# Optimization experiments

Measured on AMD Instinct MI355X. Metric: run time of the kernel, lower is better.

Reference implementation:

```python
import jax, jax.numpy as jnp
import numpy as np
from jax import lax

B, N, IN_DIM = 8, 196, 2048
C = 256          # conv_channels / subspace dim
G = 1            # relation_glimpse


def _dilated_conv(x, w, b, dil):
    # x: [B,N,N,Cin], w: [3,3,Cin,Cout], SAME padding, rhs dilation per source
    y = lax.conv_general_dilated(x, w, window_strides=(1, 1), padding='SAME',
                                 rhs_dilation=dil,
                                 dimension_numbers=('NHWC', 'HWIO', 'NHWC'))
    return y + b


def _rel_map(X):
    # X: [B,N,N,G] -> symmetric add, move glimpse to axis 1, softmax over N*N
    Xs = X + jnp.transpose(X, (0, 2, 1, 3))          # [B,N,N,G]
    m = jnp.transpose(Xs, (0, 3, 2, 1))              # [B,G,N,N]
    bsz, g, n, _ = m.shape
    m = jax.nn.softmax(m.reshape(bsz, g, n * n), axis=2)
    return m.reshape(bsz, g, n, n)


def setup_inputs() -> dict:
    key = jax.random.key(0)
    ks = jax.random.split(key, 8)
    s = lambda *sh: 1.0 / np.sqrt(sh[-2] if len(sh) > 1 else sh[0])
    return {
        'x': jax.random.normal(ks[0], (B, N, IN_DIM), jnp.float32),
        'w_prj': jax.random.normal(ks[1], (IN_DIM, C), jnp.float32) * 0.02,
        'b_prj': jnp.zeros((C,), jnp.float32),
        'w01': jax.random.normal(ks[2], (C, C // 2), jnp.float32) * 0.06,
        'b01': jnp.zeros((C // 2,), jnp.float32),
        'w02': jax.random.normal(ks[3], (C // 2, C // 4), jnp.float32) * 0.09,
        'b02': jnp.zeros((C // 4,), jnp.float32),
        'w03': jax.random.normal(ks[4], (C // 4, G), jnp.float32) * 0.125,
        'b03': jnp.zeros((G,), jnp.float32),
        'w1': jax.random.normal(ks[5], (3, 3, C, C // 2), jnp.float32) * 0.02,
        'b1': jnp.zeros((C // 2,), jnp.float32),
        'w2': jax.random.normal(ks[6], (3, 3, C // 2, C // 4), jnp.float32) * 0.03,
        'b2': jnp.zeros((C // 4,), jnp.float32),
        'w3': jax.random.normal(ks[7], (3, 3, C // 4, G), jnp.float32) * 0.04,
        'b3': jnp.zeros((G,), jnp.float32),
    }


def reference(x, w_prj, b_prj, w01, b01, w02, b02, w03, b03,
              w1, b1, w2, b2, w3, b3):
    # project to subspace: [B,N,C]
    sub = jnp.einsum('bnd,dc->bnc', x, w_prj) + b_prj
    # pairwise outer product: pair[b,i,j,c] = sub[b,i,c]*sub[b,j,c]
    pair = sub[:, :, None, :] * sub[:, None, :, :]          # [B,N,N,C]

    # branch 0: stacked 1x1 convs (pointwise) with relu; dropout = identity (eval)
    X0 = jax.nn.relu(jnp.einsum('bijc,cd->bijd', pair, w01) + b01)
    X0 = jax.nn.relu(jnp.einsum('bijc,cd->bijd', X0, w02) + b02)
    X0 = jax.nn.relu(jnp.einsum('bijc,cd->bijd', X0, w03) + b03)  # [B,N,N,G]
    rel_map0 = _rel_map(X0)                                  # [B,G,N,N]

    # branch 1: stacked 3x3 dilated convs, dilations (1,1),(1,2),(1,4)
    X1 = jax.nn.relu(_dilated_conv(pair, w1, b1, (1, 1)))
    X1 = jax.nn.relu(_dilated_conv(X1, w2, b2, (1, 2)))
    X1 = jax.nn.relu(_dilated_conv(X1, w3, b3, (1, 4)))      # [B,N,N,G]
    rel_map1 = _rel_map(X1)

    # aggregation over glimpses: rel_x = sum_g (map1[g]@x + map0[g]@x) / (2G)
    rel_x = (jnp.einsum('bgij,bjd->bid', rel_map1, x) +
             jnp.einsum('bgij,bjd->bid', rel_map0, x)) / (2.0 * G)
    return rel_x.reshape(x.shape[0], -1)                     # [B, N*in_dim]
```

## Files before the change

### kernel.cpp

```cpp
#include <hip/hip_runtime.h>
#include <cmath>

#define N_TOK 196
#define NPX   38416
#define CDIM  256

typedef _Float16 f16;
typedef __attribute__((ext_vector_type(8))) _Float16 half8;
typedef __attribute__((ext_vector_type(4))) float f32x4;

__global__ __launch_bounds__(256) void gemm_prj(
    const float* __restrict__ x,
    const float* __restrict__ wp,
    float* __restrict__ P)
{
    __shared__ f16 As[64 * 40];
    __shared__ f16 Bs[64 * 40];
    int tid = threadIdx.x;
    int m0 = blockIdx.y * 64, n0 = blockIdx.x * 64;
    int kz = blockIdx.z;
    int wave = tid >> 6, lane = tid & 63;
    int quad = lane >> 4, l16 = lane & 15;
    f32x4 zero = {0.f, 0.f, 0.f, 0.f};
    f32x4 acc[4] = {zero, zero, zero, zero};

    for (int k0 = kz * 512; k0 < kz * 512 + 512; k0 += 32) {
        __syncthreads();
        for (int e = tid; e < 2048; e += 256) {
            int m = e >> 5, kk = e & 31;
            int gm = m0 + m;
            float v = (gm < 1568) ? x[(size_t)gm * 2048 + k0 + kk] : 0.f;
            As[m * 40 + kk] = (f16)v;
        }
        for (int e = tid; e < 2048; e += 256) {
            int kk = e >> 6, n = e & 63;
            Bs[n * 40 + kk] = (f16)wp[(size_t)(k0 + kk) * 256 + n0 + n];
        }
        __syncthreads();
        half8 a = *(const half8*)(As + (wave * 16 + l16) * 40 + quad * 8);
        #pragma unroll
        for (int nt = 0; nt < 4; ++nt) {
            half8 bf = *(const half8*)(Bs + (nt * 16 + l16) * 40 + quad * 8);
            acc[nt] = __builtin_amdgcn_mfma_f32_16x16x32_f16(a, bf, acc[nt], 0, 0, 0);
        }
    }
    float* Pz = P + (size_t)kz * 401408;
    int mb = m0 + wave * 16 + quad * 4;
    #pragma unroll
    for (int nt = 0; nt < 4; ++nt) {
        int gn = n0 + nt * 16 + l16;
        #pragma unroll
        for (int r = 0; r < 4; ++r) {
            int gm = mb + r;
            if (gm < 1568) Pz[(size_t)gm * 256 + gn] = acc[nt][r];
        }
    }
}

__global__ void reduce_subh(const float* __restrict__ P,
                            const float* __restrict__ bias,
                            f16* __restrict__ subh)
{
    int e = blockIdx.x * 256 + threadIdx.x;
    if (e >= 401408) return;
    float s = bias[e & 255];
    #pragma unroll
    for (int z = 0; z < 4; ++z) s += P[(size_t)z * 401408 + e];
    subh[e] = (f16)s;
}

__device__ __forceinline__ void frag_pack(const float* w, f16* wf,
                                          int Kc, int D, int e)
{
    int tiles = D >> 4, kch = Kc >> 5;
    int lane = e & 63;
    int rest = e >> 6;
    int k = rest % kch; rest /= kch;
    int tile = rest % tiles;
    int tap = rest / tiles;
    int l16 = lane & 15, quad = lane >> 4;
    const float* src = w + ((size_t)tap * Kc + k * 32 + quad * 8) * D + tile * 16 + l16;
    f16* dst = wf + (size_t)e * 8;
    #pragma unroll
    for (int j = 0; j < 8; ++j) dst[j] = (f16)src[(size_t)j * D];
}

__global__ void cvt_all(const float* __restrict__ w1, const float* __restrict__ w2,
                        const float* __restrict__ w01, const float* __restrict__ w02,
                        f16* __restrict__ w1f, f16* __restrict__ w2f,
                        f16* __restrict__ w01t, f16* __restrict__ w02t)
{
    int blk = blockIdx.x, tid = threadIdx.x;
    if (blk < 144) {
        int e = blk * 256 + tid;
        frag_pack(w1, w1f, 256, 128, e);
    } else if (blk < 180) {
        int e = (blk - 144) * 256 + tid;
        frag_pack(w2, w2f, 128, 64, e);
    } else if (blk < 308) {
        int e = (blk - 180) * 256 + tid;
        int c = e >> 7, d = e & 127;
        w01t[(size_t)d * 256 + c] = (f16)w01[e];
    } else {
        int e = (blk - 308) * 256 + tid;
        int c = e >> 6, d = e & 63;
        w02t[(size_t)d * 128 + c] = (f16)w02[e];
    }
}

__global__ __launch_bounds__(256) void cvt_xT(const float* __restrict__ x,
                                              f16* __restrict__ xht)
{
    __shared__ float t[32][33];
    int b = blockIdx.z;
    int i0 = blockIdx.y * 32, n0 = blockIdx.x * 32;
    const float* xb = x + (size_t)b * 196 * 2048;
    for (int e = threadIdx.x; e < 1024; e += 256) {
        int r = e >> 5, c = e & 31;
        int gi = i0 + r;
        t[r][c] = (gi < 196) ? xb[(size_t)gi * 2048 + n0 + c] : 0.f;
    }
    __syncthreads();
    f16* xb2 = xht + (size_t)b * 2048 * 200;
    for (int e = threadIdx.x; e < 1024; e += 256) {
        int nl = e >> 5, il = e & 31;
        int gi = i0 + il, gn = n0 + nl;
        if (gi < 200) xb2[(size_t)gn * 200 + gi] = (f16)t[il][nl];
    }
}

__global__ __launch_bounds__(256, 2) void conv1_mfma(
    const f16* __restrict__ sub_h,
    const f16* __restrict__ w1f,
    const float* __restrict__ b1,
    f16* __restrict__ Y1h)
{
    __shared__ f16 sh[17408];
    f16* SJ = sh;
    f16* SI = sh + 8976;
    f16* OT = sh;

    int b = blockIdx.z;
    int i0 = blockIdx.y * 8, j0 = blockIdx.x * 32;
    int tid = threadIdx.x;
    const f16* subB = sub_h + (size_t)b * N_TOK * CDIM;

    uint4 zz = make_uint4(0, 0, 0, 0);
    for (int e = tid; e < 1088; e += 256) {
        int r = e >> 5, q = e & 31;
        int gj = j0 - 1 + r;
        uint4 v = zz;
        if (gj >= 0 && gj < N_TOK) v = *(const uint4*)(subB + gj * CDIM + q * 8);
        *(uint4*)(SJ + r * 264 + q * 8) = v;
    }
    for (int e = tid; e < 320; e += 256) {
        int r = e >> 5, q = e & 31;
        int gi = i0 - 1 + r;
        uint4 v = zz;
        if (gi >= 0 && gi < N_TOK) v = *(const uint4*)(subB + gi * CDIM + q * 8);
        *(uint4*)(SI + r * 264 + q * 8) = v;
    }
    __syncthreads();

    int wave = tid >> 6, lane = tid & 63;
    int quad = lane >> 4, l16 = lane & 15;
    int p  = wave >> 1;
    int dh = wave & 1;
    int d0 = dh * 64;

    float bias_r[4];
    #pragma unroll
    for (int n = 0; n < 4; ++n) bias_r[n] = b1[d0 + n * 16 + l16];

    const f16* wbase = w1f + (size_t)lane * 8 + (size_t)dh * 4 * 4096;

    f32x4 zero = {0.f, 0.f, 0.f, 0.f};
    f32x4 acc[8][4];
    #pragma unroll
    for (int m = 0; m < 8; ++m)
        #pragma unroll
        for (int n = 0; n < 4; ++n) acc[m][n] = zero;

    for (int k = 0; k < 8; ++k) {
        int c0 = k * 32;
        half8 si[6];
        #pragma unroll
        for (int r = 0; r < 6; ++r)
            si[r] = *(const half8*)(SI + (p * 4 + r) * 264 + c0 + quad * 8);
        half8 sj[2][3];
        #pragma unroll
        for (int jf = 0; jf < 2; ++jf)
            #pragma unroll
            for (int dd = 0; dd < 3; ++dd)
                sj[jf][dd] = *(const half8*)(SJ + (jf * 16 + l16 + dd) * 264 + c0 + quad * 8);

        #pragma unroll
        for (int dj = 0; dj < 3; ++dj) {
            half8 bf[3][4];
            #pragma unroll
            for (int di = 0; di < 3; ++di)
                #pragma unroll
                for (int n = 0; n < 4; ++n)
                    bf[di][n] = *(const half8*)(wbase + (size_t)(di * 3 + dj) * 32768
                                                + n * 4096 + k * 512);
            #pragma unroll
            for (int r = 0; r < 6; ++r) {
                half8 a0 = si[r] * sj[0][dj];
                half8 a1 = si[r] * sj[1][dj];
                #pragma unroll
                for (int di = 0; di < 3; ++di) {
                    int i = r - di;
                    if (i < 0 || i > 3) continue;
                    #pragma unroll
                    for (int n = 0; n < 4; ++n) {
                        acc[i * 2 + 0][n] = __builtin_amdgcn_mfma_f32_16x16x32_f16(
                            a0, bf[di][n], acc[i * 2 + 0][n], 0, 0, 0);
                        acc[i * 2 + 1][n] = __builtin_amdgcn_mfma_f32_16x16x32_f16(
                            a1, bf[di][n], acc[i * 2 + 1][n], 0, 0, 0);
                    }
                }
            }
        }
    }

    __syncthreads();
    f16* Yb = Y1h + (size_t)b * NPX * 128;
    #pragma unroll
    for (int ph = 0; ph < 2; ++ph) {
        if (p == ph) {
            #pragma unroll
            for (int i = 0; i < 4; ++i)
                #pragma unroll
                for (int jf = 0; jf < 2; ++jf) {
                    int m = i * 2 + jf;
                    #pragma unroll
                    for (int n = 0; n < 4; ++n) {
                        int dl = d0 + n * 16 + l16;
                        #pragma unroll
                        for (int r = 0; r < 4; ++r) {
                            int pxl = i * 32 + jf * 16 + quad * 4 + r;
                            OT[pxl * 136 + dl] = (f16)fmaxf(acc[m][n][r] + bias_r[n], 0.f);
                        }
                    }
                }
        }
        __syncthreads();
        for (int e = tid; e < 2048; e += 256) {
            int pxl = e >> 4, q = e & 15;
            int gi = i0 + ph * 4 + (pxl >> 5), gj = j0 + (pxl & 31);
            if (gi < N_TOK && gj < N_TOK)
                *(uint4*)(Yb + ((size_t)gi * N_TOK + gj) * 128 + q * 8) =
                    *(const uint4*)(OT + pxl * 136 + q * 8);
        }
        __syncthreads();
    }
}

__global__ __launch_bounds__(256, 2) void conv2_mfma(
    const f16* __restrict__ Y1h, const f16* __restrict__ w2f,
    const float* __restrict__ b2, f16* __restrict__ Y2h)
{
    __shared__ f16 sh[19584];
    f16* Ys = sh;
    f16* OT = sh;

    int b = blockIdx.z;
    int i0 = blockIdx.y * 2, j0 = blockIdx.x * 32;
    int tid = threadIdx.x;
    const f16* Yb = Y1h + (size_t)b * NPX * 128;

    uint4 zz = make_uint4(0, 0, 0, 0);
    for (int e = tid; e < 2304; e += 256) {
        int ir = e / 576, rem = e - ir * 576;
        int jq = rem >> 4, q = rem & 15;
        int gi = i0 - 1 + ir, gj = j0 - 2 + jq;
        uint4 v = zz;
        if (gi >= 0 && gi < N_TOK && gj >= 0 && gj < N_TOK)
            v = *(const uint4*)(Yb + ((size_t)gi * N_TOK + gj) * 128 + q * 8);
        *(uint4*)(Ys + (ir * 36 + jq) * 136 + q * 8) = v;
    }
    __syncthreads();

    int wave = tid >> 6, lane = tid & 63;
    int quad = lane >> 4, l16 = lane & 15;
    int ii = wave >> 1, jb = (wave & 1) * 16;

    const f16* wbase = w2f + (size_t)lane * 8;

    f32x4 zero = {0.f, 0.f, 0.f, 0.f};
    f32x4 acc[4] = {zero, zero, zero, zero};

    #pragma unroll
    for (int tap = 0; tap < 9; ++tap) {
        int di = tap / 3 - 1, dj2 = (tap % 3 - 1) * 2;
        #pragma unroll
        for (int k = 0; k < 4; ++k) {
            int c0 = k * 32;
            half8 a = *(const half8*)(Ys + ((ii + di + 1) * 36 + jb + l16 + dj2 + 2) * 136
                                      + c0 + quad * 8);
            #pragma unroll
            for (int n = 0; n < 4; ++n) {
                half8 bf = *(const half8*)(wbase + (size_t)tap * 8192 + n * 2048 + k * 512);
                acc[n] = __builtin_amdgcn_mfma_f32_16x16x32_f16(a, bf, acc[n], 0, 0, 0);
            }
        }
    }
    __syncthreads();
    #pragma unroll
    for (int n = 0; n < 4; ++n) {
        int d = n * 16 + l16;
        float bias = b2[d];
        #pragma unroll
        for (int r = 0; r < 4; ++r) {
            int px = ii * 32 + jb + quad * 4 + r;
            OT[px * 72 + d] = (f16)fmaxf(acc[n][r] + bias, 0.f);
        }
    }
    __syncthreads();
    f16* Zb = Y2h + (size_t)b * NPX * 64;
    for (int e = tid; e < 512; e += 256) {
        int px = e >> 3, q = e & 7;
        int i = i0 + (px >> 5), j = j0 + (px & 31);
        if (j < N_TOK)
            *(uint4*)(Zb + ((size_t)i * N_TOK + j) * 64 + q * 8) =
                *(const uint4*)(OT + px * 72 + q * 8);
    }
}

__global__ __launch_bounds__(256) void conv3_h(
    const f16* __restrict__ Y2h, const float* __restrict__ w3,
    const float* __restrict__ b3, float* __restrict__ X1)
{
    __shared__ float w[576];
    int b = blockIdx.y;
    const f16* Yb = Y2h + (size_t)b * NPX * 64;
    for (int e = threadIdx.x; e < 576; e += 256) w[e] = w3[e];
    __syncthreads();
    int px = blockIdx.x * 256 + threadIdx.x;
    if (px >= NPX) return;
    int i = px / 196, j = px - i * 196;
    float s = b3[0];
    for (int tap = 0; tap < 9; ++tap) {
        int gi = i + tap / 3 - 1, gj = j + (tap % 3 - 1) * 4;
        if (gi < 0 || gi >= N_TOK || gj < 0 || gj >= N_TOK) continue;
        const half8* src = (const half8*)(Yb + ((size_t)gi * N_TOK + gj) * 64);
        const float* wt = w + tap * 64;
        #pragma unroll
        for (int q = 0; q < 8; ++q) {
            half8 h = src[q];
            #pragma unroll
            for (int e = 0; e < 8; ++e) s += (float)h[e] * wt[q * 8 + e];
        }
    }
    X1[(size_t)b * NPX + px] = fmaxf(s, 0.f);
}

__global__ __launch_bounds__(256, 2) void branch0_mfma(
    const f16* __restrict__ sub_h,
    const f16* __restrict__ w01t,
    const float* __restrict__ b01,
    const f16* __restrict__ w02t,
    const float* __restrict__ b02,
    const float* __restrict__ w03, const float* __restrict__ b03,
    float* __restrict__ X0)
{
    __shared__ f16 sh[32000];
    __shared__ float W3s[64];
    f16* SJ = sh;
    f16* SI = sh + 8448;
    f16* BW = sh + 9472;
    f16* H1 = sh + 14592;
    f16* H2 = sh;

    int b = blockIdx.z;
    int i0 = blockIdx.y * 4, j0 = blockIdx.x * 32;
    int tid = threadIdx.x;
    const f16* subB = sub_h + (size_t)b * N_TOK * CDIM;

    uint4 zz = make_uint4(0, 0, 0, 0);
    for (int e = tid; e < 1024; e += 256) {
        int r = e >> 5, q = e & 31;
        int gj = j0 + r;
        uint4 v = zz;
        if (gj < N_TOK) v = *(const uint4*)(subB + gj * CDIM + q * 8);
        *(uint4*)(SJ + r * 264 + q * 8) = v;
    }
    if (tid < 128) {
        int r = tid >> 5, q = tid & 31;
        int gi = i0 + r;
        uint4 v = zz;
        if (gi < N_TOK) v = *(const uint4*)(subB + gi * CDIM + q * 8);
        *(uint4*)(SI + r * 256 + q * 8) = v;
    }
    if (tid < 64) W3s[tid] = w03[tid];

    int wave = tid >> 6, lane = tid & 63;
    int quad = lane >> 4, l16 = lane & 15;
    int ii = wave;

    f32x4 zero = {0.f, 0.f, 0.f, 0.f};
    f32x4 acc[2][8];
    #pragma unroll
    for (int t = 0; t < 2; ++t)
        #pragma unroll
        for (int n = 0; n < 8; ++n) acc[t][n] = zero;

    for (int c0 = 0; c0 < 256; c0 += 32) {
        __syncthreads();
        for (int e = tid; e < 512; e += 256) {
            int d = e >> 2, q = e & 3;
            *(uint4*)(BW + d * 40 + q * 8) =
                *(const uint4*)(w01t + (size_t)d * 256 + c0 + q * 8);
        }
        __syncthreads();
        half8 sib = *(const half8*)(SI + ii * 256 + c0 + quad * 8);
        half8 a0 = sib * *(const half8*)(SJ + l16 * 264 + c0 + quad * 8);
        half8 a1 = sib * *(const half8*)(SJ + (l16 + 16) * 264 + c0 + quad * 8);
        #pragma unroll
        for (int n = 0; n < 8; ++n) {
            half8 bf = *(const half8*)(BW + (n * 16 + l16) * 40 + quad * 8);
            acc[0][n] = __builtin_amdgcn_mfma_f32_16x16x32_f16(a0, bf, acc[0][n], 0, 0, 0);
            acc[1][n] = __builtin_amdgcn_mfma_f32_16x16x32_f16(a1, bf, acc[1][n], 0, 0, 0);
        }
    }
    #pragma unroll
    for (int t = 0; t < 2; ++t)
        #pragma unroll
        for (int n = 0; n < 8; ++n) {
            int d = n * 16 + l16;
            float bias = b01[d];
            #pragma unroll
            for (int r = 0; r < 4; ++r) {
                int px = ii * 32 + t * 16 + quad * 4 + r;
                H1[px * 136 + d] = (f16)fmaxf(acc[t][n][r] + bias, 0.f);
            }
        }

    f32x4 acc2[2][4];
    #pragma unroll
    for (int t = 0; t < 2; ++t)
        #pragma unroll
        for (int n = 0; n < 4; ++n) acc2[t][n] = zero;

    for (int c0 = 0; c0 < 128; c0 += 32) {
        __syncthreads();
        {
            int d = tid >> 2, q = tid & 3;
            if (d < 64)
                *(uint4*)(BW + d * 40 + q * 8) =
                    *(const uint4*)(w02t + (size_t)d * 128 + c0 + q * 8);
        }
        __syncthreads();
        half8 a0 = *(const half8*)(H1 + (ii * 32 + l16) * 136 + c0 + quad * 8);
        half8 a1 = *(const half8*)(H1 + (ii * 32 + 16 + l16) * 136 + c0 + quad * 8);
        #pragma unroll
        for (int n = 0; n < 4; ++n) {
            half8 bf = *(const half8*)(BW + (n * 16 + l16) * 40 + quad * 8);
            acc2[0][n] = __builtin_amdgcn_mfma_f32_16x16x32_f16(a0, bf, acc2[0][n], 0, 0, 0);
            acc2[1][n] = __builtin_amdgcn_mfma_f32_16x16x32_f16(a1, bf, acc2[1][n], 0, 0, 0);
        }
    }
    #pragma unroll
    for (int t = 0; t < 2; ++t)
        #pragma unroll
        for (int n = 0; n < 4; ++n) {
            int e = n * 16 + l16;
            float bias = b02[e];
            #pragma unroll
            for (int r = 0; r < 4; ++r) {
                int px = ii * 32 + t * 16 + quad * 4 + r;
                H2[px * 72 + e] = (f16)fmaxf(acc2[t][n][r] + bias, 0.f);
            }
        }
    __syncthreads();
    if (tid < 128) {
        int px = tid;
        float s = b03[0];
        const f16* h = H2 + px * 72;
        #pragma unroll 8
        for (int c = 0; c < 64; ++c) s += (float)h[c] * W3s[c];
        int i = i0 + (px >> 5), j = j0 + (px & 31);
        if (j < N_TOK)
            X0[(size_t)b * NPX + i * N_TOK + j] = fmaxf(s, 0.f);
    }
}

__global__ __launch_bounds__(1024) void symsoftmax(float* __restrict__ X0,
                                                   float* __restrict__ X1)
{
    __shared__ float red[32];
    __shared__ float red2[32];
    float* X = (blockIdx.y ? X1 : X0) + (long long)blockIdx.x * NPX;
    int tid = threadIdx.x;
    float v[38];
    float mx = -3.0e38f;
    #pragma unroll
    for (int p = 0; p < 38; ++p) {
        int e = tid + p * 1024;
        if (e < NPX) {
            int i = e / 196, j = e - i * 196;
            float t = X[e] + X[j * 196 + i];
            v[p] = t;
            mx = fmaxf(mx, t);
        } else v[p] = -3.0e38f;
    }
    #pragma unroll
    for (int off = 32; off > 0; off >>= 1) mx = fmaxf(mx, __shfl_xor(mx, off));
    if ((tid & 63) == 0) red[tid >> 6] = mx;
    __syncthreads();
    if (tid < 64) {
        float m = (tid < 16) ? red[tid] : -3.0e38f;
        #pragma unroll
        for (int off = 8; off > 0; off >>= 1) m = fmaxf(m, __shfl_xor(m, off));
        if (tid == 0) red[0] = m;
    }
    __syncthreads();
    mx = red[0];
    float s = 0.f;
    #pragma unroll
    for (int p = 0; p < 38; ++p) {
        int e = tid + p * 1024;
        float ex = (e < NPX) ? expf(v[p] - mx) : 0.f;
        v[p] = ex;
        s += ex;
    }
    #pragma unroll
    for (int off = 32; off > 0; off >>= 1) s += __shfl_xor(s, off);
    if ((tid & 63) == 0) red2[tid >> 6] = s;
    __syncthreads();
    if (tid < 64) {
        float m = (tid < 16) ? red2[tid] : 0.f;
        #pragma unroll
        for (int off = 8; off > 0; off >>= 1) m += __shfl_xor(m, off);
        if (tid == 0) red2[0] = m;
    }
    __syncthreads();
    float scale = 0.5f / red2[0];
    #pragma unroll
    for (int p = 0; p < 38; ++p) {
        int e = tid + p * 1024;
        if (e < NPX) X[e] = v[p] * scale;
    }
}

__global__ void combine_ph(const float* __restrict__ X0,
                           const float* __restrict__ X1,
                           f16* __restrict__ Ph)
{
    int e = blockIdx.x * 256 + threadIdx.x;
    if (e >= 8 * 196 * 200) return;
    int j = e % 200;
    int row = e / 200;
    f16 v = (f16)0.f;
    if (j < 196) {
        int src = row * 196 + j;
        v = (f16)((X0[src] + X1[src]) * 512.0f);
    }
    Ph[e] = v;
}

__global__ __launch_bounds__(256, 2) void gemm_out(
    const f16* __restrict__ Ph, const f16* __restrict__ xht,
    float* __restrict__ out)
{
    __shared__ f16 As[64 * 72];
    __shared__ f16 Bs[128 * 72];
    int b = blockIdx.z;
    int n0 = blockIdx.x * 128, m0 = blockIdx.y * 64;
    int tid = threadIdx.x;
    const f16* Pb = Ph + (size_t)b * 196 * 200;
    const f16* xb = xht + (size_t)b * 2048 * 200;

    int wave = tid >> 6, lane = tid & 63;
    int quad = lane >> 4, l16 = lane & 15;

    f32x4 zero = {0.f, 0.f, 0.f, 0.f};
    f32x4 acc[8];
    #pragma unroll
    for (int n = 0; n < 8; ++n) acc[n] = zero;

    uint4 zz = make_uint4(0, 0, 0, 0);
    for (int k0 = 0; k0 < 256; k0 += 64) {
        __syncthreads();
        for (int e = tid; e < 512; e += 256) {
            int r = e >> 3, q = e & 7;
            int gm = m0 + r, k = k0 + q * 8;
            uint4 v = zz;
            if (gm < 196 && k < 200) v = *(const uint4*)(Pb + (size_t)gm * 200 + k);
            *(uint4*)(As + r * 72 + q * 8) = v;
        }
        for (int e = tid; e < 1024; e += 256) {
            int r = e >> 3, q = e & 7;
            int k = k0 + q * 8;
            uint4 v = zz;
            if (k < 200) v = *(const uint4*)(xb + (size_t)(n0 + r) * 200 + k);
            *(uint4*)(Bs + r * 72 + q * 8) = v;
        }
        __syncthreads();
        #pragma unroll
        for (int ks = 0; ks < 2; ++ks) {
            half8 a = *(const half8*)(As + (wave * 16 + l16) * 72 + ks * 32 + quad * 8);
            #pragma unroll
            for (int n = 0; n < 8; ++n) {
                half8 bf = *(const half8*)(Bs + (n * 16 + l16) * 72 + ks * 32 + quad * 8);
                acc[n] = __builtin_amdgcn_mfma_f32_16x16x32_f16(a, bf, acc[n], 0, 0, 0);
            }
        }
    }
    int m_base = m0 + wave * 16 + quad * 4;
    float* ob = out + (size_t)b * 196 * 2048;
    #pragma unroll
    for (int n = 0; n < 8; ++n) {
        int gn = n0 + n * 16 + l16;
        #pragma unroll
        for (int r = 0; r < 4; ++r) {
            int gm = m_base + r;
            if (gm < 196) ob[(size_t)gm * 2048 + gn] = acc[n][r] * (1.0f / 512.0f);
        }
    }
}

extern "C" void kernel_launch(void* const* d_in, const int* in_sizes, int n_in,
                              void* d_out, int out_size, void* d_ws, size_t ws_size,
                              hipStream_t stream)
{
    (void)in_sizes; (void)n_in; (void)out_size; (void)ws_size;
    const float* x     = (const float*)d_in[0];
    const float* w_prj = (const float*)d_in[1];
    const float* b_prj = (const float*)d_in[2];
    const float* w01   = (const float*)d_in[3];
    const float* b01   = (const float*)d_in[4];
    const float* w02   = (const float*)d_in[5];
    const float* b02   = (const float*)d_in[6];
    const float* w03   = (const float*)d_in[7];
    const float* b03   = (const float*)d_in[8];
    const float* w1    = (const float*)d_in[9];
    const float* b1    = (const float*)d_in[10];
    const float* w2    = (const float*)d_in[11];
    const float* b2    = (const float*)d_in[12];
    const float* w3    = (const float*)d_in[13];
    const float* b3    = (const float*)d_in[14];

    char* W = (char*)d_ws;
    float* part = (float*)(W + 0);
    float* X0   = (float*)(W + 12845056);
    float* X1   = (float*)(W + 14074368);
    f16*   subh = (f16*)(W + 15303680);
    f16*   w1f  = (f16*)(W + 16106496);
    f16*   w2f  = (f16*)(W + 16696320);
    f16*   w01t = (f16*)(W + 16843776);
    f16*   w02t = (f16*)(W + 16909312);
    f16*   Ph   = (f16*)(W + 16925696);
    f16*   xht  = (f16*)(W + 17552896);
    f16*   Y1h  = (f16*)(W + 24106496);
    f16*   Y2h  = (f16*)(W + 102782464);

    gemm_prj<<<dim3(4, 25, 4), 256, 0, stream>>>(x, w_prj, part);
    reduce_subh<<<dim3(1568), 256, 0, stream>>>(part, b_prj, subh);

    cvt_all<<<dim3(340), 256, 0, stream>>>(w1, w2, w01, w02, w1f, w2f, w01t, w02t);
    cvt_xT<<<dim3(64, 7, 8), 256, 0, stream>>>(x, xht);

    branch0_mfma<<<dim3(7, 49, 8), 256, 0, stream>>>(
        subh, w01t, b01, w02t, b02, w03, b03, X0);

    conv1_mfma<<<dim3(7, 25, 8), 256, 0, stream>>>(subh, w1f, b1, Y1h);
    conv2_mfma<<<dim3(7, 98, 8), 256, 0, stream>>>(Y1h, w2f, b2, Y2h);
    conv3_h<<<dim3(151, 8), 256, 0, stream>>>(Y2h, w3, b3, X1);

    symsoftmax<<<dim3(8, 2), 1024, 0, stream>>>(X0, X1);

    combine_ph<<<dim3(1225), 256, 0, stream>>>(X0, X1, Ph);

    gemm_out<<<dim3(16, 4, 8), 256, 0, stream>>>(Ph, xht, (float*)d_out);
}
```

Baseline: 569.0 us.

## Merge launches: fuse conv1 with branch0, xT into cvt_all, combine into gemm_out

Branch0 and conv1 now run as two block ranges of one launch, and the x transpose moves into the weight-conversion kernel. The combine step is folded into the A-tile load of the output GEMM, which removes the Ph intermediate buffer. conv3 stores its weights in f16 and uses fdot2. The aim is fewer kernel launches, more concurrency between the two independent branches, and one less full pass over memory. The cost is heterogeneous blocks in one grid with larger shared memory, plus scalar fp32 loads in the gemm_out A-tile path.

```diff
diff --git a/kernel.cpp b/kernel.cpp
--- a/kernel.cpp
+++ b/kernel.cpp
@@ -6,12 +6,12 @@
 #define CDIM  256
 
 typedef _Float16 f16;
+typedef __attribute__((ext_vector_type(2))) _Float16 half2_t;
 typedef __attribute__((ext_vector_type(8))) _Float16 half8;
 typedef __attribute__((ext_vector_type(4))) float f32x4;
 
 __global__ __launch_bounds__(256) void gemm_prj(
-    const float* __restrict__ x,
-    const float* __restrict__ wp,
+    const float* __restrict__ x, const float* __restrict__ wp,
     float* __restrict__ P)
 {
     __shared__ f16 As[64 * 40];
@@ -87,172 +87,285 @@
 
 __global__ void cvt_all(const float* __restrict__ w1, const float* __restrict__ w2,
                         const float* __restrict__ w01, const float* __restrict__ w02,
+                        const float* __restrict__ x,
                         f16* __restrict__ w1f, f16* __restrict__ w2f,
-                        f16* __restrict__ w01t, f16* __restrict__ w02t)
-{
+                        f16* __restrict__ w01t, f16* __restrict__ w02t,
+                        f16* __restrict__ xht)
+{
+    __shared__ float t[32][33];
     int blk = blockIdx.x, tid = threadIdx.x;
     if (blk < 144) {
-        int e = blk * 256 + tid;
-        frag_pack(w1, w1f, 256, 128, e);
+        frag_pack(w1, w1f, 256, 128, blk * 256 + tid);
     } else if (blk < 180) {
-        int e = (blk - 144) * 256 + tid;
-        frag_pack(w2, w2f, 128, 64, e);
+        frag_pack(w2, w2f, 128, 64, (blk - 144) * 256 + tid);
     } else if (blk < 308) {
         int e = (blk - 180) * 256 + tid;
         int c = e >> 7, d = e & 127;
         w01t[(size_t)d * 256 + c] = (f16)w01[e];
-    } else {
+    } else if (blk < 340) {
         int e = (blk - 308) * 256 + tid;
         int c = e >> 6, d = e & 63;
         w02t[(size_t)d * 128 + c] = (f16)w02[e];
-    }
-}
-
-__global__ __launch_bounds__(256) void cvt_xT(const float* __restrict__ x,
-                                              f16* __restrict__ xht)
-{
-    __shared__ float t[32][33];
+    } else {
+        int l = blk - 340;
+        int b = l / 448, rem = l % 448;
+        int i0 = (rem >> 6) * 32, n0 = (rem & 63) * 32;
+        const float* xb = x + (size_t)b * 196 * 2048;
+        for (int e = tid; e < 1024; e += 256) {
+            int r = e >> 5, c = e & 31;
+            int gi = i0 + r;
+            t[r][c] = (gi < 196) ? xb[(size_t)gi * 2048 + n0 + c] : 0.f;
+        }
+        __syncthreads();
+        f16* xb2 = xht + (size_t)b * 2048 * 200;
+        for (int e = tid; e < 1024; e += 256) {
+            int nl = e >> 5, il = e & 31;
+            int gi = i0 + il, gn = n0 + nl;
+            if (gi < 200) xb2[(size_t)gn * 200 + gi] = (f16)t[il][nl];
+        }
+    }
+}
+
+__global__ __launch_bounds__(256, 2) void stage1(
+    const f16* __restrict__ sub_h,
+    const f16* __restrict__ w1f, const float* __restrict__ b1,
+    f16* __restrict__ Y1h,
+    const f16* __restrict__ w01t, const float* __restrict__ b01,
+    const f16* __restrict__ w02t, const float* __restrict__ b02,
+    const float* __restrict__ w03, const float* __restrict__ b03,
+    float* __restrict__ X0)
+{
+    __shared__ f16 sh[32064];
+    __shared__ float W3s[64];
     int b = blockIdx.z;
-    int i0 = blockIdx.y * 32, n0 = blockIdx.x * 32;
-    const float* xb = x + (size_t)b * 196 * 2048;
-    for (int e = threadIdx.x; e < 1024; e += 256) {
-        int r = e >> 5, c = e & 31;
-        int gi = i0 + r;
-        t[r][c] = (gi < 196) ? xb[(size_t)gi * 2048 + n0 + c] : 0.f;
-    }
-    __syncthreads();
-    f16* xb2 = xht + (size_t)b * 2048 * 200;
-    for (int e = threadIdx.x; e < 1024; e += 256) {
-        int nl = e >> 5, il = e & 31;
-        int gi = i0 + il, gn = n0 + nl;
-        if (gi < 200) xb2[(size_t)gn * 200 + gi] = (f16)t[il][nl];
-    }
-}
-
-__global__ __launch_bounds__(256, 2) void conv1_mfma(
-    const f16* __restrict__ sub_h,
-    const f16* __restrict__ w1f,
-    const float* __restrict__ b1,
-    f16* __restrict__ Y1h)
-{
-    __shared__ f16 sh[17408];
-    f16* SJ = sh;
-    f16* SI = sh + 8976;
-    f16* OT = sh;
-
-    int b = blockIdx.z;
-    int i0 = blockIdx.y * 8, j0 = blockIdx.x * 32;
     int tid = threadIdx.x;
     const f16* subB = sub_h + (size_t)b * N_TOK * CDIM;
-
     uint4 zz = make_uint4(0, 0, 0, 0);
-    for (int e = tid; e < 1088; e += 256) {
-        int r = e >> 5, q = e & 31;
-        int gj = j0 - 1 + r;
-        uint4 v = zz;
-        if (gj >= 0 && gj < N_TOK) v = *(const uint4*)(subB + gj * CDIM + q * 8);
-        *(uint4*)(SJ + r * 264 + q * 8) = v;
-    }
-    for (int e = tid; e < 320; e += 256) {
-        int r = e >> 5, q = e & 31;
-        int gi = i0 - 1 + r;
-        uint4 v = zz;
-        if (gi >= 0 && gi < N_TOK) v = *(const uint4*)(subB + gi * CDIM + q * 8);
-        *(uint4*)(SI + r * 264 + q * 8) = v;
-    }
-    __syncthreads();
-
     int wave = tid >> 6, lane = tid & 63;
     int quad = lane >> 4, l16 = lane & 15;
-    int p  = wave >> 1;
-    int dh = wave & 1;
-    int d0 = dh * 64;
-
-    float bias_r[4];
-    #pragma unroll
-    for (int n = 0; n < 4; ++n) bias_r[n] = b1[d0 + n * 16 + l16];
-
-    const f16* wbase = w1f + (size_t)lane * 8 + (size_t)dh * 4 * 4096;
-
-    f32x4 zero = {0.f, 0.f, 0.f, 0.f};
-    f32x4 acc[8][4];
-    #pragma unroll
-    for (int m = 0; m < 8; ++m)
-        #pragma unroll
-        for (int n = 0; n < 4; ++n) acc[m][n] = zero;
-
-    for (int k = 0; k < 8; ++k) {
-        int c0 = k * 32;
-        half8 si[6];
-        #pragma unroll
-        for (int r = 0; r < 6; ++r)
-            si[r] = *(const half8*)(SI + (p * 4 + r) * 264 + c0 + quad * 8);
-        half8 sj[2][3];
-        #pragma unroll
-        for (int jf = 0; jf < 2; ++jf)
-            #pragma unroll
-            for (int dd = 0; dd < 3; ++dd)
-                sj[jf][dd] = *(const half8*)(SJ + (jf * 16 + l16 + dd) * 264 + c0 + quad * 8);
-
-        #pragma unroll
-        for (int dj = 0; dj < 3; ++dj) {
-            half8 bf[3][4];
-            #pragma unroll
-            for (int di = 0; di < 3; ++di)
+
+    if (blockIdx.y < 25) {
+        f16* SJ = sh;
+        f16* SI = sh + 8976;
+        f16* OT = sh;
+        int i0 = blockIdx.y * 8, j0 = blockIdx.x * 32;
+
+        for (int e = tid; e < 1088; e += 256) {
+            int r = e >> 5, q = e & 31;
+            int gj = j0 - 1 + r;
+            uint4 v = zz;
+            if (gj >= 0 && gj < N_TOK) v = *(const uint4*)(subB + gj * CDIM + q * 8);
+            *(uint4*)(SJ + r * 264 + q * 8) = v;
+        }
+        for (int e = tid; e < 320; e += 256) {
+            int r = e >> 5, q = e & 31;
+            int gi = i0 - 1 + r;
+            uint4 v = zz;
+            if (gi >= 0 && gi < N_TOK) v = *(const uint4*)(subB + gi * CDIM + q * 8);
+            *(uint4*)(SI + r * 264 + q * 8) = v;
+        }
+        __syncthreads();
+
+        int p  = wave >> 1;
+        int dh = wave & 1;
+        int d0 = dh * 64;
+
+        float bias_r[4];
+        #pragma unroll
+        for (int n = 0; n < 4; ++n) bias_r[n] = b1[d0 + n * 16 + l16];
+
+        const f16* wbase = w1f + (size_t)lane * 8 + (size_t)dh * 4 * 4096;
+
+        f32x4 zero = {0.f, 0.f, 0.f, 0.f};
+        f32x4 acc[8][4];
+        #pragma unroll
+        for (int m = 0; m < 8; ++m)
+            #pragma unroll
+            for (int n = 0; n < 4; ++n) acc[m][n] = zero;
+
+        for (int k = 0; k < 8; ++k) {
+            int c0 = k * 32;
+            half8 si[6];
+            #pragma unroll
+            for (int r = 0; r < 6; ++r)
+                si[r] = *(const half8*)(SI + (p * 4 + r) * 264 + c0 + quad * 8);
+            half8 sj[2][3];
+            #pragma unroll
+            for (int jf = 0; jf < 2; ++jf)
                 #pragma unroll
-                for (int n = 0; n < 4; ++n)
-                    bf[di][n] = *(const half8*)(wbase + (size_t)(di * 3 + dj) * 32768
-                                                + n * 4096 + k * 512);
-            #pragma unroll
-            for (int r = 0; r < 6; ++r) {
-                half8 a0 = si[r] * sj[0][dj];
-                half8 a1 = si[r] * sj[1][dj];
+                for (int dd = 0; dd < 3; ++dd)
+                    sj[jf][dd] = *(const half8*)(SJ + (jf * 16 + l16 + dd) * 264 + c0 + quad * 8);
+
+            #pragma unroll
+            for (int dj = 0; dj < 3; ++dj) {
+                half8 bf[3][4];
                 #pragma unroll
-                for (int di = 0; di < 3; ++di) {
-                    int i = r - di;
-                    if (i < 0 || i > 3) continue;
+                for (int di = 0; di < 3; ++di)
                     #pragma unroll
-                    for (int n = 0; n < 4; ++n) {
-                        acc[i * 2 + 0][n] = __builtin_amdgcn_mfma_f32_16x16x32_f16(
-                            a0, bf[di][n], acc[i * 2 + 0][n], 0, 0, 0);
-                        acc[i * 2 + 1][n] = __builtin_amdgcn_mfma_f32_16x16x32_f16(
-                            a1, bf[di][n], acc[i * 2 + 1][n], 0, 0, 0);
-                    }
-                }
-            }
-        }
-    }
-
-    __syncthreads();
-    f16* Yb = Y1h + (size_t)b * NPX * 128;
-    #pragma unroll
-    for (int ph = 0; ph < 2; ++ph) {
-        if (p == ph) {
-            #pragma unroll
-            for (int i = 0; i < 4; ++i)
+                    for (int n = 0; n < 4; ++n)
+                        bf[di][n] = *(const half8*)(wbase + (size_t)(di * 3 + dj) * 32768
+                                                    + n * 4096 + k * 512);
                 #pragma unroll
-                for (int jf = 0; jf < 2; ++jf) {
-                    int m = i * 2 + jf;
+                for (int r = 0; r < 6; ++r) {
+                    half8 a0 = si[r] * sj[0][dj];
+                    half8 a1 = si[r] * sj[1][dj];
                     #pragma unroll
-                    for (int n = 0; n < 4; ++n) {
-                        int dl = d0 + n * 16 + l16;
+                    for (int di = 0; di < 3; ++di) {
+                        int i = r - di;
+                        if (i < 0 || i > 3) continue;
                         #pragma unroll
-                        for (int r = 0; r < 4; ++r) {
-                            int pxl = i * 32 + jf * 16 + quad * 4 + r;
-                            OT[pxl * 136 + dl] = (f16)fmaxf(acc[m][n][r] + bias_r[n], 0.f);
+                        for (int n = 0; n < 4; ++n) {
+                            acc[i * 2 + 0][n] = __builtin_amdgcn_mfma_f32_16x16x32_f16(
+                                a0, bf[di][n], acc[i * 2 + 0][n], 0, 0, 0);
+                            acc[i * 2 + 1][n] = __builtin_amdgcn_mfma_f32_16x16x32_f16(
+                                a1, bf[di][n], acc[i * 2 + 1][n], 0, 0, 0);
                         }
                     }
                 }
-        }
-        __syncthreads();
-        for (int e = tid; e < 2048; e += 256) {
-            int pxl = e >> 4, q = e & 15;
-            int gi = i0 + ph * 4 + (pxl >> 5), gj = j0 + (pxl & 31);
-            if (gi < N_TOK && gj < N_TOK)
-                *(uint4*)(Yb + ((size_t)gi * N_TOK + gj) * 128 + q * 8) =
-                    *(const uint4*)(OT + pxl * 136 + q * 8);
-        }
-        __syncthreads();
+            }
+        }
+
+        __syncthreads();
+        f16* Yb = Y1h + (size_t)b * NPX * 128;
+        #pragma unroll
+        for (int ph = 0; ph < 2; ++ph) {
+            if (p == ph) {
+                #pragma unroll
+                for (int i = 0; i < 4; ++i)
+                    #pragma unroll
+                    for (int jf = 0; jf < 2; ++jf) {
+                        int m = i * 2 + jf;
+                        #pragma unroll
+                        for (int n = 0; n < 4; ++n) {
+                            int dl = d0 + n * 16 + l16;
+                            #pragma unroll
+                            for (int r = 0; r < 4; ++r) {
+                                int pxl = i * 32 + jf * 16 + quad * 4 + r;
+                                OT[pxl * 136 + dl] = (f16)fmaxf(acc[m][n][r] + bias_r[n], 0.f);
+                            }
+                        }
+                    }
+            }
+            __syncthreads();
+            for (int e = tid; e < 2048; e += 256) {
+                int pxl = e >> 4, q = e & 15;
+                int gi = i0 + ph * 4 + (pxl >> 5), gj = j0 + (pxl & 31);
+                if (gi < N_TOK && gj < N_TOK)
+                    *(uint4*)(Yb + ((size_t)gi * N_TOK + gj) * 128 + q * 8) =
+                        *(const uint4*)(OT + pxl * 136 + q * 8);
+            }
+            __syncthreads();
+        }
+    } else {
+        f16* SJ = sh;
+        f16* SI = sh + 8448;
+        f16* BW = sh + 9472;
+        f16* H1 = sh + 14592;
+        f16* H2 = sh;
+        int i0 = (blockIdx.y - 25) * 4, j0 = blockIdx.x * 32;
+
+        for (int e = tid; e < 1024; e += 256) {
+            int r = e >> 5, q = e & 31;
+            int gj = j0 + r;
+            uint4 v = zz;
+            if (gj < N_TOK) v = *(const uint4*)(subB + gj * CDIM + q * 8);
+            *(uint4*)(SJ + r * 264 + q * 8) = v;
+        }
+        if (tid < 128) {
+            int r = tid >> 5, q = tid & 31;
+            int gi = i0 + r;
+            uint4 v = zz;
+            if (gi < N_TOK) v = *(const uint4*)(subB + gi * CDIM + q * 8);
+            *(uint4*)(SI + r * 256 + q * 8) = v;
+        }
+        if (tid < 64) W3s[tid] = w03[tid];
+
+        int ii = wave;
+        f32x4 zero = {0.f, 0.f, 0.f, 0.f};
+        f32x4 acc[2][8];
+        #pragma unroll
+        for (int t = 0; t < 2; ++t)
+            #pragma unroll
+            for (int n = 0; n < 8; ++n) acc[t][n] = zero;
+
+        for (int c0 = 0; c0 < 256; c0 += 32) {
+            __syncthreads();
+            for (int e = tid; e < 512; e += 256) {
+                int d = e >> 2, q = e & 3;
+                *(uint4*)(BW + d * 40 + q * 8) =
+                    *(const uint4*)(w01t + (size_t)d * 256 + c0 + q * 8);
+            }
+            __syncthreads();
+            half8 sib = *(const half8*)(SI + ii * 256 + c0 + quad * 8);
+            half8 a0 = sib * *(const half8*)(SJ + l16 * 264 + c0 + quad * 8);
+            half8 a1 = sib * *(const half8*)(SJ + (l16 + 16) * 264 + c0 + quad * 8);
+            #pragma unroll
+            for (int n = 0; n < 8; ++n) {
+                half8 bf = *(const half8*)(BW + (n * 16 + l16) * 40 + quad * 8);
+                acc[0][n] = __builtin_amdgcn_mfma_f32_16x16x32_f16(a0, bf, acc[0][n], 0, 0, 0);
+                acc[1][n] = __builtin_amdgcn_mfma_f32_16x16x32_f16(a1, bf, acc[1][n], 0, 0, 0);
+            }
+        }
+        #pragma unroll
+        for (int t = 0; t < 2; ++t)
+            #pragma unroll
+            for (int n = 0; n < 8; ++n) {
+                int d = n * 16 + l16;
+                float bias = b01[d];
+                #pragma unroll
+                for (int r = 0; r < 4; ++r) {
+                    int px = ii * 32 + t * 16 + quad * 4 + r;
+                    H1[px * 136 + d] = (f16)fmaxf(acc[t][n][r] + bias, 0.f);
+                }
+            }
+
+        f32x4 acc2[2][4];
+        #pragma unroll
+        for (int t = 0; t < 2; ++t)
+            #pragma unroll
+            for (int n = 0; n < 4; ++n) acc2[t][n] = zero;
+
+        for (int c0 = 0; c0 < 128; c0 += 32) {
+            __syncthreads();
+            {
+                int d = tid >> 2, q = tid & 3;
+                if (d < 64)
+                    *(uint4*)(BW + d * 40 + q * 8) =
+                        *(const uint4*)(w02t + (size_t)d * 128 + c0 + q * 8);
+            }
+            __syncthreads();
+            half8 a0 = *(const half8*)(H1 + (ii * 32 + l16) * 136 + c0 + quad * 8);
+            half8 a1 = *(const half8*)(H1 + (ii * 32 + 16 + l16) * 136 + c0 + quad * 8);
+            #pragma unroll
+            for (int n = 0; n < 4; ++n) {
+                half8 bf = *(const half8*)(BW + (n * 16 + l16) * 40 + quad * 8);
+                acc2[0][n] = __builtin_amdgcn_mfma_f32_16x16x32_f16(a0, bf, acc2[0][n], 0, 0, 0);
+                acc2[1][n] = __builtin_amdgcn_mfma_f32_16x16x32_f16(a1, bf, acc2[1][n], 0, 0, 0);
+            }
+        }
+        #pragma unroll
+        for (int t = 0; t < 2; ++t)
+            #pragma unroll
+            for (int n = 0; n < 4; ++n) {
+                int e = n * 16 + l16;
+                float bias = b02[e];
+                #pragma unroll
+                for (int r = 0; r < 4; ++r) {
+                    int px = ii * 32 + t * 16 + quad * 4 + r;
+                    H2[px * 72 + e] = (f16)fmaxf(acc2[t][n][r] + bias, 0.f);
+                }
+            }
+        __syncthreads();
+        if (tid < 128) {
+            int px = tid;
+            float s = b03[0];
+            const f16* h = H2 + px * 72;
+            #pragma unroll 8
+            for (int c = 0; c < 64; ++c) s += (float)h[c] * W3s[c];
+            int i = i0 + (px >> 5), j = j0 + (px & 31);
+            if (j < N_TOK)
+                X0[(size_t)b * NPX + i * N_TOK + j] = fmaxf(s, 0.f);
+        }
     }
 }
 
@@ -331,10 +444,10 @@
     const f16* __restrict__ Y2h, const float* __restrict__ w3,
     const float* __restrict__ b3, float* __restrict__ X1)
 {
-    __shared__ float w[576];
+    __shared__ f16 wh[576];
     int b = blockIdx.y;
     const f16* Yb = Y2h + (size_t)b * NPX * 64;
-    for (int e = threadIdx.x; e < 576; e += 256) w[e] = w3[e];
+    for (int e = threadIdx.x; e < 576; e += 256) wh[e] = (f16)w3[e];
     __syncthreads();
     int px = blockIdx.x * 256 + threadIdx.x;
     if (px >= NPX) return;
@@ -344,145 +457,27 @@
         int gi = i + tap / 3 - 1, gj = j + (tap % 3 - 1) * 4;
         if (gi < 0 || gi >= N_TOK || gj < 0 || gj >= N_TOK) continue;
         const half8* src = (const half8*)(Yb + ((size_t)gi * N_TOK + gj) * 64);
-        const float* wt = w + tap * 64;
+        const half8* wt8 = (const half8*)(wh + tap * 64);
         #pragma unroll
         for (int q = 0; q < 8; ++q) {
             half8 h = src[q];
-            #pragma unroll
-            for (int e = 0; e < 8; ++e) s += (float)h[e] * wt[q * 8 + e];
+            half8 w8 = wt8[q];
+#if defined(__has_builtin) && __has_builtin(__builtin_amdgcn_fdot2)
+            s = __builtin_amdgcn_fdot2(__builtin_shufflevector(h, h, 0, 1),
+                                       __builtin_shufflevector(w8, w8, 0, 1), s, false);
+            s = __builtin_amdgcn_fdot2(__builtin_shufflevector(h, h, 2, 3),
+                                       __builtin_shufflevector(w8, w8, 2, 3), s, false);
+            s = __builtin_amdgcn_fdot2(__builtin_shufflevector(h, h, 4, 5),
+                                       __builtin_shufflevector(w8, w8, 4, 5), s, false);
+            s = __builtin_amdgcn_fdot2(__builtin_shufflevector(h, h, 6, 7),
+                                       __builtin_shufflevector(w8, w8, 6, 7), s, false);
+#else
+            #pragma unroll
+            for (int e = 0; e < 8; ++e) s += (float)h[e] * (float)w8[e];
+#endif
         }
     }
     X1[(size_t)b * NPX + px] = fmaxf(s, 0.f);
-}
-
-__global__ __launch_bounds__(256, 2) void branch0_mfma(
-    const f16* __restrict__ sub_h,
-    const f16* __restrict__ w01t,
-    const float* __restrict__ b01,
-    const f16* __restrict__ w02t,
-    const float* __restrict__ b02,
-    const float* __restrict__ w03, const float* __restrict__ b03,
-    float* __restrict__ X0)
-{
-    __shared__ f16 sh[32000];
-    __shared__ float W3s[64];
-    f16* SJ = sh;
-    f16* SI = sh + 8448;
-    f16* BW = sh + 9472;
-    f16* H1 = sh + 14592;
-    f16* H2 = sh;
-
-    int b = blockIdx.z;
-    int i0 = blockIdx.y * 4, j0 = blockIdx.x * 32;
-    int tid = threadIdx.x;
-    const f16* subB = sub_h + (size_t)b * N_TOK * CDIM;
-
-    uint4 zz = make_uint4(0, 0, 0, 0);
-    for (int e = tid; e < 1024; e += 256) {
-        int r = e >> 5, q = e & 31;
-        int gj = j0 + r;
-        uint4 v = zz;
-        if (gj < N_TOK) v = *(const uint4*)(subB + gj * CDIM + q * 8);
-        *(uint4*)(SJ + r * 264 + q * 8) = v;
-    }
-    if (tid < 128) {
-        int r = tid >> 5, q = tid & 31;
-        int gi = i0 + r;
-        uint4 v = zz;
-        if (gi < N_TOK) v = *(const uint4*)(subB + gi * CDIM + q * 8);
-        *(uint4*)(SI + r * 256 + q * 8) = v;
-    }
-    if (tid < 64) W3s[tid] = w03[tid];
-
-    int wave = tid >> 6, lane = tid & 63;
-    int quad = lane >> 4, l16 = lane & 15;
-    int ii = wave;
-
-    f32x4 zero = {0.f, 0.f, 0.f, 0.f};
-    f32x4 acc[2][8];
-    #pragma unroll
-    for (int t = 0; t < 2; ++t)
-        #pragma unroll
-        for (int n = 0; n < 8; ++n) acc[t][n] = zero;
-
-    for (int c0 = 0; c0 < 256; c0 += 32) {
-        __syncthreads();
-        for (int e = tid; e < 512; e += 256) {
-            int d = e >> 2, q = e & 3;
-            *(uint4*)(BW + d * 40 + q * 8) =
-                *(const uint4*)(w01t + (size_t)d * 256 + c0 + q * 8);
-        }
-        __syncthreads();
-        half8 sib = *(const half8*)(SI + ii * 256 + c0 + quad * 8);
-        half8 a0 = sib * *(const half8*)(SJ + l16 * 264 + c0 + quad * 8);
-        half8 a1 = sib * *(const half8*)(SJ + (l16 + 16) * 264 + c0 + quad * 8);
-        #pragma unroll
-        for (int n = 0; n < 8; ++n) {
-            half8 bf = *(const half8*)(BW + (n * 16 + l16) * 40 + quad * 8);
-            acc[0][n] = __builtin_amdgcn_mfma_f32_16x16x32_f16(a0, bf, acc[0][n], 0, 0, 0);
-            acc[1][n] = __builtin_amdgcn_mfma_f32_16x16x32_f16(a1, bf, acc[1][n], 0, 0, 0);
-        }
-    }
-    #pragma unroll
-    for (int t = 0; t < 2; ++t)
-        #pragma unroll
-        for (int n = 0; n < 8; ++n) {
-            int d = n * 16 + l16;
-            float bias = b01[d];
-            #pragma unroll
-            for (int r = 0; r < 4; ++r) {
-                int px = ii * 32 + t * 16 + quad * 4 + r;
-                H1[px * 136 + d] = (f16)fmaxf(acc[t][n][r] + bias, 0.f);
-            }
-        }
-
-    f32x4 acc2[2][4];
-    #pragma unroll
-    for (int t = 0; t < 2; ++t)
-        #pragma unroll
-        for (int n = 0; n < 4; ++n) acc2[t][n] = zero;
-
-    for (int c0 = 0; c0 < 128; c0 += 32) {
-        __syncthreads();
-        {
-            int d = tid >> 2, q = tid & 3;
-            if (d < 64)
-                *(uint4*)(BW + d * 40 + q * 8) =
-                    *(const uint4*)(w02t + (size_t)d * 128 + c0 + q * 8);
-        }
-        __syncthreads();
-        half8 a0 = *(const half8*)(H1 + (ii * 32 + l16) * 136 + c0 + quad * 8);
-        half8 a1 = *(const half8*)(H1 + (ii * 32 + 16 + l16) * 136 + c0 + quad * 8);
-        #pragma unroll
-        for (int n = 0; n < 4; ++n) {
-            half8 bf = *(const half8*)(BW + (n * 16 + l16) * 40 + quad * 8);
-            acc2[0][n] = __builtin_amdgcn_mfma_f32_16x16x32_f16(a0, bf, acc2[0][n], 0, 0, 0);
-            acc2[1][n] = __builtin_amdgcn_mfma_f32_16x16x32_f16(a1, bf, acc2[1][n], 0, 0, 0);
-        }
-    }
-    #pragma unroll
-    for (int t = 0; t < 2; ++t)
-        #pragma unroll
-        for (int n = 0; n < 4; ++n) {
-            int e = n * 16 + l16;
-            float bias = b02[e];
-            #pragma unroll
-            for (int r = 0; r < 4; ++r) {
-                int px = ii * 32 + t * 16 + quad * 4 + r;
-                H2[px * 72 + e] = (f16)fmaxf(acc2[t][n][r] + bias, 0.f);
-            }
-        }
-    __syncthreads();
-    if (tid < 128) {
-        int px = tid;
-        float s = b03[0];
-        const f16* h = H2 + px * 72;
-        #pragma unroll 8
-        for (int c = 0; c < 64; ++c) s += (float)h[c] * W3s[c];
-        int i = i0 + (px >> 5), j = j0 + (px & 31);
-        if (j < N_TOK)
-            X0[(size_t)b * NPX + i * N_TOK + j] = fmaxf(s, 0.f);
-    }
 }
 
 __global__ __launch_bounds__(1024) void symsoftmax(float* __restrict__ X0,
@@ -543,32 +538,15 @@
     }
 }
 
-__global__ void combine_ph(const float* __restrict__ X0,
-                           const float* __restrict__ X1,
-                           f16* __restrict__ Ph)
-{
-    int e = blockIdx.x * 256 + threadIdx.x;
-    if (e >= 8 * 196 * 200) return;
-    int j = e % 200;
-    int row = e / 200;
-    f16 v = (f16)0.f;
-    if (j < 196) {
-        int src = row * 196 + j;
-        v = (f16)((X0[src] + X1[src]) * 512.0f);
-    }
-    Ph[e] = v;
-}
-
 __global__ __launch_bounds__(256, 2) void gemm_out(
-    const f16* __restrict__ Ph, const f16* __restrict__ xht,
-    float* __restrict__ out)
+    const float* __restrict__ X0, const float* __restrict__ X1,
+    const f16* __restrict__ xht, float* __restrict__ out)
 {
     __shared__ f16 As[64 * 72];
     __shared__ f16 Bs[128 * 72];
     int b = blockIdx.z;
     int n0 = blockIdx.x * 128, m0 = blockIdx.y * 64;
     int tid = threadIdx.x;
-    const f16* Pb = Ph + (size_t)b * 196 * 200;
     const f16* xb = xht + (size_t)b * 2048 * 200;
 
     int wave = tid >> 6, lane = tid & 63;
@@ -584,10 +562,19 @@
         __syncthreads();
         for (int e = tid; e < 512; e += 256) {
             int r = e >> 3, q = e & 7;
-            int gm = m0 + r, k = k0 + q * 8;
-            uint4 v = zz;
-            if (gm < 196 && k < 200) v = *(const uint4*)(Pb + (size_t)gm * 200 + k);
-            *(uint4*)(As + r * 72 + q * 8) = v;
+            int gm = m0 + r, kb = k0 + q * 8;
+            f16 tmp[8];
+            #pragma unroll
+            for (int t = 0; t < 8; ++t) {
+                int k = kb + t;
+                float v = 0.f;
+                if (gm < 196 && k < 196) {
+                    size_t src = (size_t)b * NPX + (size_t)gm * 196 + k;
+                    v = (X0[src] + X1[src]) * 512.0f;
+                }
+                tmp[t] = (f16)v;
+            }
+            *(uint4*)(As + r * 72 + q * 8) = *(const uint4*)tmp;
         }
         for (int e = tid; e < 1024; e += 256) {
             int r = e >> 3, q = e & 7;
@@ -650,7 +637,6 @@
     f16*   w2f  = (f16*)(W + 16696320);
     f16*   w01t = (f16*)(W + 16843776);
     f16*   w02t = (f16*)(W + 16909312);
-    f16*   Ph   = (f16*)(W + 16925696);
     f16*   xht  = (f16*)(W + 17552896);
     f16*   Y1h  = (f16*)(W + 24106496);
     f16*   Y2h  = (f16*)(W + 102782464);
@@ -658,19 +644,16 @@
     gemm_prj<<<dim3(4, 25, 4), 256, 0, stream>>>(x, w_prj, part);
     reduce_subh<<<dim3(1568), 256, 0, stream>>>(part, b_prj, subh);
 
-    cvt_all<<<dim3(340), 256, 0, stream>>>(w1, w2, w01, w02, w1f, w2f, w01t, w02t);
-    cvt_xT<<<dim3(64, 7, 8), 256, 0, stream>>>(x, xht);
-
-    branch0_mfma<<<dim3(7, 49, 8), 256, 0, stream>>>(
-        subh, w01t, b01, w02t, b02, w03, b03, X0);
-
-    conv1_mfma<<<dim3(7, 25, 8), 256, 0, stream>>>(subh, w1f, b1, Y1h);
+    cvt_all<<<dim3(3924), 256, 0, stream>>>(w1, w2, w01, w02, x,
+                                            w1f, w2f, w01t, w02t, xht);
+
+    stage1<<<dim3(7, 74, 8), 256, 0, stream>>>(
+        subh, w1f, b1, Y1h, w01t, b01, w02t, b02, w03, b03, X0);
+
     conv2_mfma<<<dim3(7, 98, 8), 256, 0, stream>>>(Y1h, w2f, b2, Y2h);
     conv3_h<<<dim3(151, 8), 256, 0, stream>>>(Y2h, w3, b3, X1);
 
     symsoftmax<<<dim3(8, 2), 1024, 0, stream>>>(X0, X1);
 
-    combine_ph<<<dim3(1225), 256, 0, stream>>>(X0, X1, Ph);
-
-    gemm_out<<<dim3(16, 4, 8), 256, 0, stream>>>(Ph, xht, (float*)d_out);
-}
+    gemm_out<<<dim3(16, 4, 8), 256, 0, stream>>>(X0, X1, xht, (float*)d_out);
+}
```

Measured after the change: 573.1 us. No clear change (+0.7%).
